# Kernel tuning notes

Measured on AMD Instinct MI355X. Metric: run time of the kernel, lower is better.

Reference implementation:

```python
import jax, jax.numpy as jnp
import numpy as np

B = 32; H = 56; W = 56; DIM = 192; WS = 7; SHIFT = 3; HEADS = 6
HEAD_DIM = DIM // HEADS; N = WS * WS; NW = (H // WS) * (W // WS)
HIDDEN = int(DIM * 4.0)
EPS = 1e-5


def _rel_pos_index():
    # standard Swin relative position index, shape (N, N), static
    coords = np.stack(np.meshgrid(np.arange(WS), np.arange(WS), indexing='ij'))  # (2, ws, ws)
    coords = coords.reshape(2, -1)                                               # (2, N)
    rel = (coords[:, :, None] - coords[:, None, :]).transpose(1, 2, 0)           # (N, N, 2)
    rel[:, :, 0] += WS - 1
    rel[:, :, 1] += WS - 1
    rel[:, :, 0] *= 2 * WS - 1
    return rel.sum(-1)  # (N, N)

REL_IDX = _rel_pos_index()


def _compute_attn_mask():
    # standard Swin SW-MSA mask, shape (NW, N, N), static
    img = np.zeros((H, W), dtype=np.float32)
    cnt = 0
    slices = (slice(0, -WS), slice(-WS, -SHIFT), slice(-SHIFT, None))
    for hs in slices:
        for ws_ in slices:
            img[hs, ws_] = cnt
            cnt += 1
    mw = img.reshape(H // WS, WS, W // WS, WS).transpose(0, 2, 1, 3).reshape(-1, N)  # (NW, N)
    diff = mw[:, None, :] - mw[:, :, None]
    return np.where(diff != 0, np.float32(-100.0), np.float32(0.0))


def _layernorm(x, g, b):
    mu = jnp.mean(x, axis=-1, keepdims=True)
    var = jnp.mean(jnp.square(x - mu), axis=-1, keepdims=True)
    return (x - mu) * jax.lax.rsqrt(var + EPS) * g + b


def setup_inputs() -> dict:
    key = jax.random.key(0)
    ks = jax.random.split(key, 8)
    s = 0.02
    inp = {
        'x': jax.random.normal(ks[0], (B, H * W, DIM), dtype=jnp.float32),
        'g1': jnp.ones((DIM,), jnp.float32), 'b1': jnp.zeros((DIM,), jnp.float32),
        'qkv_w': jax.random.normal(ks[1], (DIM, 3 * DIM), jnp.float32) * s,
        'qkv_b': jnp.zeros((3 * DIM,), jnp.float32),
        'proj_w': jax.random.normal(ks[2], (DIM, DIM), jnp.float32) * s,
        'proj_b': jnp.zeros((DIM,), jnp.float32),
        'rel_table': jax.random.normal(ks[3], ((2 * WS - 1) ** 2, HEADS), jnp.float32) * s,
        'g2': jnp.ones((DIM,), jnp.float32), 'b2': jnp.zeros((DIM,), jnp.float32),
        'fc1_w': jax.random.normal(ks[4], (DIM, HIDDEN), jnp.float32) * s,
        'fc1_b': jnp.zeros((HIDDEN,), jnp.float32),
        'fc2_w': jax.random.normal(ks[5], (HIDDEN, DIM), jnp.float32) * s,
        'fc2_b': jnp.zeros((DIM,), jnp.float32),
        'attn_mask': jnp.asarray(_compute_attn_mask()),
    }
    return inp


def reference(x, g1, b1, qkv_w, qkv_b, proj_w, proj_b, rel_table, g2, b2,
              fc1_w, fc1_b, fc2_w, fc2_b, attn_mask):
    shortcut = x
    h = _layernorm(x, g1, b1).reshape(B, H, W, DIM)
    h = jnp.roll(h, (-SHIFT, -SHIFT), axis=(1, 2))
    # window partition -> (B*NW, N, C)
    win = h.reshape(B, H // WS, WS, W // WS, WS, DIM).transpose(0, 1, 3, 2, 4, 5)
    win = win.reshape(-1, N, DIM)
    qkv = (win @ qkv_w + qkv_b).reshape(-1, N, 3, HEADS, HEAD_DIM).transpose(2, 0, 3, 1, 4)
    q, k, v = qkv[0], qkv[1], qkv[2]                         # (B*NW, heads, N, d)
    attn = jnp.einsum('whnd,whmd->whnm', q, k) * (HEAD_DIM ** -0.5)
    bias = rel_table[REL_IDX.reshape(-1)].reshape(N, N, HEADS).transpose(2, 0, 1)
    attn = attn + bias[None]
    attn = attn.reshape(B, NW, HEADS, N, N) + attn_mask[None, :, None]
    attn = jax.nn.softmax(attn, axis=-1).reshape(-1, HEADS, N, N)
    out = jnp.einsum('whnm,whmd->whnd', attn, v).transpose(0, 2, 1, 3).reshape(-1, N, DIM)
    out = out @ proj_w + proj_b
    # window reverse -> (B, H, W, C)
    out = out.reshape(B, H // WS, W // WS, WS, WS, DIM).transpose(0, 1, 3, 2, 4, 5)
    out = out.reshape(B, H, W, DIM)
    out = jnp.roll(out, (SHIFT, SHIFT), axis=(1, 2)).reshape(B, H * W, DIM)
    x = shortcut + out
    shortcut2 = x
    h = _layernorm(x, g2, b2)
    h = jax.nn.gelu(h @ fc1_w + fc1_b, approximate=False)
    h = h @ fc2_w + fc2_b
    return shortcut2 + h
```

## Files before the change

kernel.cpp:

```cpp
#include <hip/hip_runtime.h>
#include <math.h>

#define B_      32
#define HH      56
#define WW_     56
#define DIM     192
#define WS_     7
#define SHIFT_  3
#define HEADS   6
#define HDIM    32
#define NTOK    49
#define NWIN    64
#define HIDDEN  768
#define MTOT    (B_*HH*WW_)
#define EPS_    1e-5f
#define SCALE_  0.17677669529663687f

#define ALD 200
#define PLD 40
#define VLD 72

#define MROWS 64
#define HLDQ  200

typedef unsigned short u16;
typedef __attribute__((ext_vector_type(8))) __bf16 bf16x8;
typedef __attribute__((ext_vector_type(4))) float f32x4;

__device__ __forceinline__ float bf2f(u16 u) {
    union { unsigned int i; float f; } c; c.i = ((unsigned int)u) << 16; return c.f;
}
__device__ __forceinline__ u16 f2bf(float f) {
    union { float f; unsigned int i; } c; c.f = f;
    unsigned int x = c.i;
    return (u16)((x + 0x7FFFu + ((x >> 16) & 1u)) >> 16);
}

__device__ __forceinline__ float wave_sum(float v) {
    #pragma unroll
    for (int off = 32; off > 0; off >>= 1) v += __shfl_xor(v, off, 64);
    return v;
}

__global__ __launch_bounds__(256) void transpose_w_kernel(
        const float* __restrict__ W, u16* __restrict__ Wt, int K, int N) {
    __shared__ float t[32][33];
    int nt32 = N >> 5;
    int bx = blockIdx.x % nt32;
    int by = blockIdx.x / nt32;
    int tx = threadIdx.x & 31, ty = threadIdx.x >> 5;
    #pragma unroll
    for (int i = 0; i < 4; i++)
        t[ty + i * 8][tx] = W[(size_t)(by * 32 + ty + i * 8) * N + bx * 32 + tx];
    __syncthreads();
    #pragma unroll
    for (int i = 0; i < 4; i++)
        Wt[(size_t)(bx * 32 + ty + i * 8) * K + by * 32 + tx] = f2bf(t[tx][ty + i * 8]);
}

__global__ __launch_bounds__(256) void build_tbl_kernel(
        const float* __restrict__ rel_table, const float* __restrict__ mask,
        float* __restrict__ tbl) {
    int idx = blockIdx.x * 256 + threadIdx.x;
    int kj   = idx & 63;
    int qi   = (idx >> 6) & 63;
    int head = (idx >> 12) % 6;
    int wl   = idx / (6 << 12);
    float v;
    if (qi < NTOK && kj < NTOK) {
        int qr = qi / WS_, qc = qi % WS_;
        int kr = kj / WS_, kc = kj % WS_;
        int ri = (qr - kr + 6) * 13 + (qc - kc + 6);
        v = rel_table[ri * HEADS + head] + mask[((size_t)wl * NTOK + qi) * NTOK + kj];
    } else {
        v = -1e30f;
    }
    tbl[idx] = v;
}

__global__ __launch_bounds__(256) void ln1_window_kernel(
        const float* __restrict__ x, const float* __restrict__ g,
        const float* __restrict__ b, u16* __restrict__ out) {
    int row  = blockIdx.x * 4 + (threadIdx.x >> 6);
    int lane = threadIdx.x & 63;
    int win = row / NTOK;
    int n   = row - win * NTOK;
    int bb  = win >> 6;
    int wl  = win & 63;
    int hi  = (wl >> 3) * WS_ + n / WS_;
    int hj  = (wl & 7) * WS_ + n % WS_;
    int sh = hi + SHIFT_; if (sh >= HH) sh -= HH;
    int sw = hj + SHIFT_; if (sw >= WW_) sw -= WW_;
    const float* xr = x + ((size_t)(bb * HH * WW_ + sh * WW_ + sw)) * DIM;
    float v0 = xr[lane], v1 = xr[lane + 64], v2 = xr[lane + 128];
    float s  = wave_sum(v0 + v1 + v2);
    float sq = wave_sum(v0 * v0 + v1 * v1 + v2 * v2);
    float mu  = s * (1.0f / DIM);
    float var = sq * (1.0f / DIM) - mu * mu;
    float r = rsqrtf(var + EPS_);
    u16* orow = out + (size_t)row * DIM;
    orow[lane]       = f2bf((v0 - mu) * r * g[lane]       + b[lane]);
    orow[lane + 64]  = f2bf((v1 - mu) * r * g[lane + 64]  + b[lane + 64]);
    orow[lane + 128] = f2bf((v2 - mu) * r * g[lane + 128] + b[lane + 128]);
}

__global__ __launch_bounds__(256) void ln2_kernel(
        const float* __restrict__ x, const float* __restrict__ g,
        const float* __restrict__ b, u16* __restrict__ out) {
    int row  = blockIdx.x * 4 + (threadIdx.x >> 6);
    int lane = threadIdx.x & 63;
    const float* xr = x + (size_t)row * DIM;
    float v0 = xr[lane], v1 = xr[lane + 64], v2 = xr[lane + 128];
    float s  = wave_sum(v0 + v1 + v2);
    float sq = wave_sum(v0 * v0 + v1 * v1 + v2 * v2);
    float mu  = s * (1.0f / DIM);
    float var = sq * (1.0f / DIM) - mu * mu;
    float r = rsqrtf(var + EPS_);
    u16* orow = out + (size_t)row * DIM;
    orow[lane]       = f2bf((v0 - mu) * r * g[lane]       + b[lane]);
    orow[lane + 64]  = f2bf((v1 - mu) * r * g[lane + 64]  + b[lane + 64]);
    orow[lane + 128] = f2bf((v2 - mu) * r * g[lane + 128] + b[lane + 128]);
}

__global__ __launch_bounds__(384) void fused_attn_kernel(
        const u16* __restrict__ hwin, const u16* __restrict__ qkv_wT,
        const float* __restrict__ qkv_b, const u16* __restrict__ proj_wT,
        const float* __restrict__ proj_b, const float* __restrict__ tbl,
        const float* __restrict__ x, float* __restrict__ x1) {
    __shared__ u16 sm[29184];
    u16* R1 = sm;
    u16* Vt = sm + 15360;

    const int tid  = threadIdx.x;
    const int w    = tid >> 6;
    const int lane = tid & 63;
    const int lrow = lane & 15, lq = lane >> 4;
    const int win  = blockIdx.x;
    const int wl   = win & 63, bb = win >> 6;

    {
        const uint4* src = (const uint4*)(hwin + (size_t)win * NTOK * DIM);
        uint4 z; z.x = z.y = z.z = z.w = 0u;
        #pragma unroll
        for (int it = 0; it < 4; it++) {
            int i = tid + it * 384;
            int row = i / 24, c = i - row * 24;
            uint4 v = (row < NTOK) ? src[row * 24 + c] : z;
            *(uint4*)&R1[row * ALD + c * 8] = v;
        }
    }
    __syncthreads();

    f32x4 acc[3][4][2];
    #pragma unroll
    for (int o = 0; o < 3; o++)
        #pragma unroll
        for (int mt = 0; mt < 4; mt++)
            #pragma unroll
            for (int nt = 0; nt < 2; nt++) acc[o][mt][nt] = (f32x4){0.f, 0.f, 0.f, 0.f};

    const u16* bcol[3][2];
    #pragma unroll
    for (int o = 0; o < 3; o++)
        #pragma unroll
        for (int nt = 0; nt < 2; nt++)
            bcol[o][nt] = qkv_wT + (size_t)(o * DIM + w * 32 + nt * 16 + lrow) * DIM + lq * 8;

    #pragma unroll
    for (int ks = 0; ks < 6; ks++) {
        bf16x8 aF[4];
        #pragma unroll
        for (int mt = 0; mt < 4; mt++)
            aF[mt] = *(const bf16x8*)&R1[(mt * 16 + lrow) * ALD + ks * 32 + lq * 8];
        bf16x8 bF[3][2];
        #pragma unroll
        for (int o = 0; o < 3; o++)
            #pragma unroll
            for (int nt = 0; nt < 2; nt++)
                bF[o][nt] = *(const bf16x8*)(bcol[o][nt] + ks * 32);
        __builtin_amdgcn_s_setprio(1);
        #pragma unroll
        for (int o = 0; o < 3; o++)
            #pragma unroll
            for (int mt = 0; mt < 4; mt++)
                #pragma unroll
                for (int nt = 0; nt < 2; nt++)
                    acc[o][mt][nt] = __builtin_amdgcn_mfma_f32_16x16x32_bf16(
                        aF[mt], bF[o][nt], acc[o][mt][nt], 0, 0, 0);
        __builtin_amdgcn_s_setprio(0);
    }
    float bias_[3][2];
    #pragma unroll
    for (int o = 0; o < 3; o++)
        #pragma unroll
        for (int nt = 0; nt < 2; nt++)
            bias_[o][nt] = qkv_b[o * DIM + w * 32 + nt * 16 + lrow];
    #pragma unroll
    for (int o = 0; o < 3; o++)
        #pragma unroll
        for (int mt = 0; mt < 4; mt++)
            #pragma unroll
            for (int nt = 0; nt < 2; nt++)
                #pragma unroll
                for (int r = 0; r < 4; r++) acc[o][mt][nt][r] += bias_[o][nt];

    __syncthreads();

    #pragma unroll
    for (int mt = 0; mt < 4; mt++)
        #pragma unroll
        for (int nt = 0; nt < 2; nt++)
            #pragma unroll
            for (int r = 0; r < 4; r++)
                R1[(mt * 16 + lq * 4 + r) * ALD + w * 32 + nt * 16 + lrow] =
                    f2bf(acc[0][mt][nt][r]);
    bf16x8 qf[4];
    #pragma unroll
    for (int mt = 0; mt < 4; mt++)
        qf[mt] = *(const bf16x8*)&R1[(mt * 16 + lrow) * ALD + w * 32 + lq * 8];

    #pragma unroll
    for (int mt = 0; mt < 4; mt++)
        #pragma unroll
        for (int nt = 0; nt < 2; nt++)
            #pragma unroll
            for (int r = 0; r < 4; r++)
                R1[(mt * 16 + lq * 4 + r) * ALD + w * 32 + nt * 16 + lrow] =
                    f2bf(acc[1][mt][nt][r]);
    bf16x8 kf[4];
    #pragma unroll
    for (int nt = 0; nt < 4; nt++)
        kf[nt] = *(const bf16x8*)&R1[(nt * 16 + lrow) * ALD + w * 32 + lq * 8];

    #pragma unroll
    for (int mt = 0; mt < 4; mt++)
        #pragma unroll
        for (int nt = 0; nt < 2; nt++)
            #pragma unroll
            for (int r = 0; r < 4; r++)
                Vt[(w * 32 + nt * 16 + lrow) * VLD + mt * 16 + lq * 4 + r] =
                    f2bf(acc[2][mt][nt][r]);

    f32x4 sc[4][4];
    __builtin_amdgcn_s_setprio(1);
    #pragma unroll
    for (int mt = 0; mt < 4; mt++)
        #pragma unroll
        for (int nt = 0; nt < 4; nt++) {
            f32x4 z = (f32x4){0.f, 0.f, 0.f, 0.f};
            sc[mt][nt] = __builtin_amdgcn_mfma_f32_16x16x32_bf16(qf[mt], kf[nt], z, 0, 0, 0);
        }
    __builtin_amdgcn_s_setprio(0);
    const float* tb = tbl + (((size_t)wl * HEADS + w) << 12);
    float inv[4][4];
    #pragma unroll
    for (int mt = 0; mt < 4; mt++)
        #pragma unroll
        for (int r = 0; r < 4; r++) {
            int qi = mt * 16 + lq * 4 + r;
            float mx = -3.0e38f;
            #pragma unroll
            for (int nt = 0; nt < 4; nt++) {
                float s = sc[mt][nt][r] * SCALE_ + tb[(qi << 6) + nt * 16 + lrow];
                sc[mt][nt][r] = s;
                mx = fmaxf(mx, s);
            }
            #pragma unroll
            for (int off = 8; off > 0; off >>= 1) mx = fmaxf(mx, __shfl_xor(mx, off, 64));
            float sum = 0.f;
            #pragma unroll
            for (int nt = 0; nt < 4; nt++) {
                float e = __expf(sc[mt][nt][r] - mx);
                sc[mt][nt][r] = e;
                sum += e;
            }
            #pragma unroll
            for (int off = 8; off > 0; off >>= 1) sum += __shfl_xor(sum, off, 64);
            inv[mt][r] = 1.0f / sum;
        }

    u16* Pl = R1 + w * (64 * PLD);
    f32x4 oc[4][2];
    #pragma unroll
    for (int mt = 0; mt < 4; mt++)
        #pragma unroll
        for (int nd = 0; nd < 2; nd++) oc[mt][nd] = (f32x4){0.f, 0.f, 0.f, 0.f};
    #pragma unroll
    for (int ks = 0; ks < 2; ks++) {
        #pragma unroll
        for (int mt = 0; mt < 4; mt++)
            #pragma unroll
            for (int ntl = 0; ntl < 2; ntl++)
                #pragma unroll
                for (int r = 0; r < 4; r++)
                    Pl[(mt * 16 + lq * 4 + r) * PLD + ntl * 16 + lrow] =
                        f2bf(sc[mt][ks * 2 + ntl][r]);
        bf16x8 vf[2];
        #pragma unroll
        for (int nd = 0; nd < 2; nd++)
            vf[nd] = *(const bf16x8*)&Vt[(w * 32 + nd * 16 + lrow) * VLD + ks * 32 + lq * 8];
        __builtin_amdgcn_s_setprio(1);
        #pragma unroll
        for (int mt = 0; mt < 4; mt++) {
            bf16x8 pf = *(const bf16x8*)&Pl[(mt * 16 + lrow) * PLD + lq * 8];
            #pragma unroll
            for (int nd = 0; nd < 2; nd++)
                oc[mt][nd] = __builtin_amdgcn_mfma_f32_16x16x32_bf16(pf, vf[nd],
                                                                     oc[mt][nd], 0, 0, 0);
        }
        __builtin_amdgcn_s_setprio(0);
    }
    __syncthreads();

    #pragma unroll
    for (int mt = 0; mt < 4; mt++)
        #pragma unroll
        for (int nd = 0; nd < 2; nd++)
            #pragma unroll
            for (int r = 0; r < 4; r++)
                R1[(mt * 16 + lq * 4 + r) * ALD + w * 32 + nd * 16 + lrow] =
                    f2bf(oc[mt][nd][r] * inv[mt][r]);
    __syncthreads();

    f32x4 pacc[4][2];
    #pragma unroll
    for (int mt = 0; mt < 4; mt++)
        #pragma unroll
        for (int nt = 0; nt < 2; nt++) pacc[mt][nt] = (f32x4){0.f, 0.f, 0.f, 0.f};
    const u16* pcol[2];
    #pragma unroll
    for (int nt = 0; nt < 2; nt++)
        pcol[nt] = proj_wT + (size_t)(w * 32 + nt * 16 + lrow) * DIM + lq * 8;
    #pragma unroll
    for (int ks = 0; ks < 6; ks++) {
        bf16x8 af[4];
        #pragma unroll
        for (int mt = 0; mt < 4; mt++)
            af[mt] = *(const bf16x8*)&R1[(mt * 16 + lrow) * ALD + ks * 32 + lq * 8];
        bf16x8 pb[2];
        #pragma unroll
        for (int nt = 0; nt < 2; nt++) pb[nt] = *(const bf16x8*)(pcol[nt] + ks * 32);
        __builtin_amdgcn_s_setprio(1);
        #pragma unroll
        for (int mt = 0; mt < 4; mt++)
            #pragma unroll
            for (int nt = 0; nt < 2; nt++)
                pacc[mt][nt] = __builtin_amdgcn_mfma_f32_16x16x32_bf16(
                    af[mt], pb[nt], pacc[mt][nt], 0, 0, 0);
        __builtin_amdgcn_s_setprio(0);
    }
    float pbias[2];
    #pragma unroll
    for (int nt = 0; nt < 2; nt++) pbias[nt] = proj_b[w * 32 + nt * 16 + lrow];
    #pragma unroll
    for (int mt = 0; mt < 4; mt++)
        #pragma unroll
        for (int r = 0; r < 4; r++) {
            int n = mt * 16 + lq * 4 + r;
            if (n < NTOK) {
                int hi = (wl >> 3) * WS_ + n / WS_;
                int hj = (wl & 7) * WS_ + n % WS_;
                int dh = hi + SHIFT_; if (dh >= HH) dh -= HH;
                int dw = hj + SHIFT_; if (dw >= WW_) dw -= WW_;
                size_t tok = (size_t)(bb * HH * WW_ + dh * WW_ + dw);
                #pragma unroll
                for (int nt = 0; nt < 2; nt++) {
                    int col = w * 32 + nt * 16 + lrow;
                    x1[tok * DIM + col] = x[tok * DIM + col] + pacc[mt][nt][r] + pbias[nt];
                }
            }
        }
}

__global__ __launch_bounds__(384) void mlp_fused_kernel(
        const u16* __restrict__ h2, const u16* __restrict__ fc1_wT,
        const float* __restrict__ fc1_b, const u16* __restrict__ fc2_wT,
        const float* __restrict__ fc2_b, float* __restrict__ out) {
    __shared__ u16 Ash[MROWS * ALD];
    __shared__ u16 Hsh[MROWS * HLDQ];

    const int tid  = threadIdx.x;
    const int w    = tid >> 6;
    const int lane = tid & 63;
    const int lrow = lane & 15, lq = lane >> 4;
    const int m0   = blockIdx.x * MROWS;

    {
        const uint4* src = (const uint4*)(h2 + (size_t)m0 * DIM);
        #pragma unroll
        for (int it = 0; it < 4; it++) {
            int i = tid + it * 384;
            int row = i / 24, c = i - row * 24;
            *(uint4*)&Ash[row * ALD + c * 8] = src[row * 24 + c];
        }
    }
    __syncthreads();

    f32x4 acc2[4][2];
    #pragma unroll
    for (int mt = 0; mt < 4; mt++)
        #pragma unroll
        for (int nt = 0; nt < 2; nt++) acc2[mt][nt] = (f32x4){0.f, 0.f, 0.f, 0.f};

    for (int h = 0; h < 4; h++) {
        f32x4 hacc[4][2];
        #pragma unroll
        for (int mt = 0; mt < 4; mt++)
            #pragma unroll
            for (int nt = 0; nt < 2; nt++) hacc[mt][nt] = (f32x4){0.f, 0.f, 0.f, 0.f};
        const u16* b1base = fc1_wT + (size_t)(h * 192 + w * 32) * DIM;
        #pragma unroll
        for (int ks = 0; ks < 6; ks++) {
            bf16x8 aF[4];
            #pragma unroll
            for (int mt = 0; mt < 4; mt++)
                aF[mt] = *(const bf16x8*)&Ash[(mt * 16 + lrow) * ALD + ks * 32 + lq * 8];
            bf16x8 bF[2];
            #pragma unroll
            for (int nt = 0; nt < 2; nt++)
                bF[nt] = *(const bf16x8*)(b1base + (size_t)(nt * 16 + lrow) * DIM +
                                          ks * 32 + lq * 8);
            __builtin_amdgcn_s_setprio(1);
            #pragma unroll
            for (int mt = 0; mt < 4; mt++)
                #pragma unroll
                for (int nt = 0; nt < 2; nt++)
                    hacc[mt][nt] = __builtin_amdgcn_mfma_f32_16x16x32_bf16(
                        aF[mt], bF[nt], hacc[mt][nt], 0, 0, 0);
            __builtin_amdgcn_s_setprio(0);
        }
        if (h) __syncthreads();
        #pragma unroll
        for (int nt = 0; nt < 2; nt++) {
            float bv = fc1_b[h * 192 + w * 32 + nt * 16 + lrow];
            #pragma unroll
            for (int mt = 0; mt < 4; mt++)
                #pragma unroll
                for (int r = 0; r < 4; r++) {
                    float val = hacc[mt][nt][r] + bv;
                    float gel = 0.5f * val * (1.0f + erff(val * 0.70710678118f));
                    Hsh[(mt * 16 + lq * 4 + r) * HLDQ + w * 32 + nt * 16 + lrow] = f2bf(gel);
                }
        }
        __syncthreads();

        const u16* b2base = fc2_wT + (size_t)(w * 32) * HIDDEN + h * 192;
        #pragma unroll
        for (int ks = 0; ks < 6; ks++) {
            bf16x8 hF[4];
            #pragma unroll
            for (int mt = 0; mt < 4; mt++)
                hF[mt] = *(const bf16x8*)&Hsh[(mt * 16 + lrow) * HLDQ + ks * 32 + lq * 8];
            bf16x8 b2F[2];
            #pragma unroll
            for (int nt = 0; nt < 2; nt++)
                b2F[nt] = *(const bf16x8*)(b2base + (size_t)(nt * 16 + lrow) * HIDDEN +
                                           ks * 32 + lq * 8);
            __builtin_amdgcn_s_setprio(1);
            #pragma unroll
            for (int mt = 0; mt < 4; mt++)
                #pragma unroll
                for (int nt = 0; nt < 2; nt++)
                    acc2[mt][nt] = __builtin_amdgcn_mfma_f32_16x16x32_bf16(
                        hF[mt], b2F[nt], acc2[mt][nt], 0, 0, 0);
            __builtin_amdgcn_s_setprio(0);
        }
    }

    #pragma unroll
    for (int nt = 0; nt < 2; nt++) {
        int col = w * 32 + nt * 16 + lrow;
        float bv = fc2_b[col];
        #pragma unroll
        for (int mt = 0; mt < 4; mt++)
            #pragma unroll
            for (int r = 0; r < 4; r++) {
                size_t grow = (size_t)(m0 + mt * 16 + lq * 4 + r);
                out[grow * DIM + col] = out[grow * DIM + col] + acc2[mt][nt][r] + bv;
            }
    }
}

extern "C" void kernel_launch(void* const* d_in, const int* in_sizes, int n_in,
                              void* d_out, int out_size, void* d_ws, size_t ws_size,
                              hipStream_t stream) {
    const float* x         = (const float*)d_in[0];
    const float* g1        = (const float*)d_in[1];
    const float* b1        = (const float*)d_in[2];
    const float* qkv_w     = (const float*)d_in[3];
    const float* qkv_b     = (const float*)d_in[4];
    const float* proj_w    = (const float*)d_in[5];
    const float* proj_b    = (const float*)d_in[6];
    const float* rel_table = (const float*)d_in[7];
    const float* g2        = (const float*)d_in[8];
    const float* b2        = (const float*)d_in[9];
    const float* fc1_w     = (const float*)d_in[10];
    const float* fc1_b     = (const float*)d_in[11];
    const float* fc2_w     = (const float*)d_in[12];
    const float* fc2_b     = (const float*)d_in[13];
    const float* attn_mask = (const float*)d_in[14];
    float* out = (float*)d_out;

    const size_t S = (size_t)MTOT * DIM;
    u16* wsu = (u16*)d_ws;
    u16*   hwin    = wsu;
    u16*   wT      = wsu + S;
    u16*   qkv_wT  = wT;
    u16*   proj_wT = wT + 110592;
    u16*   fc1_wT  = wT + 147456;
    u16*   fc2_wT  = wT + 294912;
    float* tbl     = (float*)(wT + 442368);

    transpose_w_kernel<<<(DIM / 32) * (3 * DIM / 32), 256, 0, stream>>>(qkv_w, qkv_wT, DIM, 3 * DIM);
    transpose_w_kernel<<<(DIM / 32) * (DIM / 32), 256, 0, stream>>>(proj_w, proj_wT, DIM, DIM);
    transpose_w_kernel<<<(DIM / 32) * (HIDDEN / 32), 256, 0, stream>>>(fc1_w, fc1_wT, DIM, HIDDEN);
    transpose_w_kernel<<<(HIDDEN / 32) * (DIM / 32), 256, 0, stream>>>(fc2_w, fc2_wT, HIDDEN, DIM);
    build_tbl_kernel<<<(NWIN * HEADS * 64 * 64) / 256, 256, 0, stream>>>(rel_table, attn_mask, tbl);

    ln1_window_kernel<<<MTOT / 4, 256, 0, stream>>>(x, g1, b1, hwin);
    fused_attn_kernel<<<B_ * NWIN, 384, 0, stream>>>(hwin, qkv_wT, qkv_b, proj_wT, proj_b,
                                                     tbl, x, out);
    ln2_kernel<<<MTOT / 4, 256, 0, stream>>>(out, g2, b2, hwin);
    mlp_fused_kernel<<<MTOT / MROWS, 384, 0, stream>>>(hwin, fc1_wT, fc1_b, fc2_wT, fc2_b, out);
}
```

Measured before the change: 502.3 us.

## Software-pipeline fused MLP with double-buffered hidden tile and prefetched fc1 weights

Restructures the fused MLP kernel so the fc1+GELU computation for the next hidden chunk runs after the fc2 accumulation of the current chunk. The hidden tile in shared memory is double-buffered, and fc1 weights for the next chunk are prefetched into registers before the fc2 phase. This removes one barrier per iteration and lets global weight loads overlap MFMA work. In exchange, shared memory use doubles (about 51KB per block) and register pressure rises from 12 extra bf16x8 fragments, which may reduce occupancy.

```diff
diff --git a/kernel.cpp b/kernel.cpp
--- a/kernel.cpp
+++ b/kernel.cpp
@@ -377,7 +377,7 @@
         const float* __restrict__ fc1_b, const u16* __restrict__ fc2_wT,
         const float* __restrict__ fc2_b, float* __restrict__ out) {
     __shared__ u16 Ash[MROWS * ALD];
-    __shared__ u16 Hsh[MROWS * HLDQ];
+    __shared__ u16 Hsh[2][MROWS * HLDQ];
 
     const int tid  = threadIdx.x;
     const int w    = tid >> 6;
@@ -402,13 +402,13 @@
         #pragma unroll
         for (int nt = 0; nt < 2; nt++) acc2[mt][nt] = (f32x4){0.f, 0.f, 0.f, 0.f};
 
-    for (int h = 0; h < 4; h++) {
+    {
         f32x4 hacc[4][2];
         #pragma unroll
         for (int mt = 0; mt < 4; mt++)
             #pragma unroll
             for (int nt = 0; nt < 2; nt++) hacc[mt][nt] = (f32x4){0.f, 0.f, 0.f, 0.f};
-        const u16* b1base = fc1_wT + (size_t)(h * 192 + w * 32) * DIM;
+        const u16* b1base = fc1_wT + (size_t)(w * 32) * DIM;
         #pragma unroll
         for (int ks = 0; ks < 6; ks++) {
             bf16x8 aF[4];
@@ -429,42 +429,96 @@
                         aF[mt], bF[nt], hacc[mt][nt], 0, 0, 0);
             __builtin_amdgcn_s_setprio(0);
         }
-        if (h) __syncthreads();
         #pragma unroll
         for (int nt = 0; nt < 2; nt++) {
-            float bv = fc1_b[h * 192 + w * 32 + nt * 16 + lrow];
+            float bv = fc1_b[w * 32 + nt * 16 + lrow];
             #pragma unroll
             for (int mt = 0; mt < 4; mt++)
                 #pragma unroll
                 for (int r = 0; r < 4; r++) {
                     float val = hacc[mt][nt][r] + bv;
                     float gel = 0.5f * val * (1.0f + erff(val * 0.70710678118f));
-                    Hsh[(mt * 16 + lq * 4 + r) * HLDQ + w * 32 + nt * 16 + lrow] = f2bf(gel);
+                    Hsh[0][(mt * 16 + lq * 4 + r) * HLDQ + w * 32 + nt * 16 + lrow] =
+                        f2bf(gel);
                 }
         }
+    }
+    __syncthreads();
+
+    for (int h = 0; h < 4; h++) {
+        bf16x8 wreg[12];
+        if (h < 3) {
+            const u16* b1base = fc1_wT + (size_t)((h + 1) * 192 + w * 32) * DIM;
+            #pragma unroll
+            for (int ks = 0; ks < 6; ks++)
+                #pragma unroll
+                for (int nt = 0; nt < 2; nt++)
+                    wreg[ks * 2 + nt] = *(const bf16x8*)(
+                        b1base + (size_t)(nt * 16 + lrow) * DIM + ks * 32 + lq * 8);
+        }
+
+        {
+            const u16* b2base = fc2_wT + (size_t)(w * 32) * HIDDEN + h * 192;
+            const u16* hb = &Hsh[h & 1][0];
+            #pragma unroll
+            for (int ks = 0; ks < 6; ks++) {
+                bf16x8 hF[4];
+                #pragma unroll
+                for (int mt = 0; mt < 4; mt++)
+                    hF[mt] = *(const bf16x8*)&hb[(mt * 16 + lrow) * HLDQ + ks * 32 + lq * 8];
+                bf16x8 b2F[2];
+                #pragma unroll
+                for (int nt = 0; nt < 2; nt++)
+                    b2F[nt] = *(const bf16x8*)(b2base + (size_t)(nt * 16 + lrow) * HIDDEN +
+                                               ks * 32 + lq * 8);
+                __builtin_amdgcn_s_setprio(1);
+                #pragma unroll
+                for (int mt = 0; mt < 4; mt++)
+                    #pragma unroll
+                    for (int nt = 0; nt < 2; nt++)
+                        acc2[mt][nt] = __builtin_amdgcn_mfma_f32_16x16x32_bf16(
+                            hF[mt], b2F[nt], acc2[mt][nt], 0, 0, 0);
+                __builtin_amdgcn_s_setprio(0);
+            }
+        }
+
+        if (h < 3) {
+            f32x4 hacc[4][2];
+            #pragma unroll
+            for (int mt = 0; mt < 4; mt++)
+                #pragma unroll
+                for (int nt = 0; nt < 2; nt++) hacc[mt][nt] = (f32x4){0.f, 0.f, 0.f, 0.f};
+            #pragma unroll
+            for (int ks = 0; ks < 6; ks++) {
+                bf16x8 aF[4];
+                #pragma unroll
+                for (int mt = 0; mt < 4; mt++)
+                    aF[mt] = *(const bf16x8*)&Ash[(mt * 16 + lrow) * ALD + ks * 32 + lq * 8];
+                __builtin_amdgcn_s_setprio(1);
+                #pragma unroll
+                for (int mt = 0; mt < 4; mt++)
+                    #pragma unroll
+                    for (int nt = 0; nt < 2; nt++)
+                        hacc[mt][nt] = __builtin_amdgcn_mfma_f32_16x16x32_bf16(
+                            aF[mt], wreg[ks * 2 + nt], hacc[mt][nt], 0, 0, 0);
+                __builtin_amdgcn_s_setprio(0);
+            }
+            u16* ho = &Hsh[(h + 1) & 1][0];
+            #pragma unroll
+            for (int nt = 0; nt < 2; nt++) {
+                float bv = fc1_b[(h + 1) * 192 + w * 32 + nt * 16 + lrow];
+                #pragma unroll
+                for (int mt = 0; mt < 4; mt++)
+                    #pragma unroll
+                    for (int r = 0; r < 4; r++) {
+                        float val = hacc[mt][nt][r] + bv;
+                        float gel = 0.5f * val * (1.0f + erff(val * 0.70710678118f));
+                        ho[(mt * 16 + lq * 4 + r) * HLDQ + w * 32 + nt * 16 + lrow] =
+                            f2bf(gel);
+                    }
+            }
+        }
         __syncthreads();
-
-        const u16* b2base = fc2_wT + (size_t)(w * 32) * HIDDEN + h * 192;
-        #pragma unroll
-        for (int ks = 0; ks < 6; ks++) {
-            bf16x8 hF[4];
-            #pragma unroll
-            for (int mt = 0; mt < 4; mt++)
-                hF[mt] = *(const bf16x8*)&Hsh[(mt * 16 + lrow) * HLDQ + ks * 32 + lq * 8];
-            bf16x8 b2F[2];
-            #pragma unroll
-            for (int nt = 0; nt < 2; nt++)
-                b2F[nt] = *(const bf16x8*)(b2base + (size_t)(nt * 16 + lrow) * HIDDEN +
-                                           ks * 32 + lq * 8);
-            __builtin_amdgcn_s_setprio(1);
-            #pragma unroll
-            for (int mt = 0; mt < 4; mt++)
-                #pragma unroll
-                for (int nt = 0; nt < 2; nt++)
-                    acc2[mt][nt] = __builtin_amdgcn_mfma_f32_16x16x32_bf16(
-                        hF[mt], b2F[nt], acc2[mt][nt], 0, 0, 0);
-            __builtin_amdgcn_s_setprio(0);
-        }
     }
 
     #pragma unroll
```

Result: slower. 554.3 us (+10.4%).
